# Optimization experiments

Measured on AMD Instinct MI355X. Metric: run time of the kernel, lower is better.

## Reference

```python
import jax, jax.numpy as jnp
import numpy as np

B, T, D, H, UNITS = 32, 2048, 512, 512, 512

def setup_inputs() -> dict:
    key = jax.random.key(0)
    ks = jax.random.split(key, 5)
    scale = 0.02
    return {
        "features": jax.random.normal(ks[0], (B, T, D), dtype=jnp.float32),
        "hidden": jax.random.normal(ks[1], (B, H), dtype=jnp.float32),
        "Wk": jax.random.normal(ks[2], (D, UNITS), dtype=jnp.float32) * scale,
        "Wb": jnp.zeros((UNITS,), dtype=jnp.float32),
        "Uk": jax.random.normal(ks[3], (H, UNITS), dtype=jnp.float32) * scale,
        "Ub": jnp.zeros((UNITS,), dtype=jnp.float32),
        "Vk": jax.random.normal(ks[4], (UNITS, 1), dtype=jnp.float32) * scale,
        "Vb": jnp.zeros((1,), dtype=jnp.float32),
    }

def reference(features, hidden, Wk, Wb, Uk, Ub, Vk, Vb):
    # features: [B, T, D], hidden: [B, H]
    wf = jnp.einsum('btd,du->btu', features, Wk) + Wb          # [B, T, U]
    uh = (hidden @ Uk + Ub)[:, None, :]                        # [B, 1, U]
    score = jnp.tanh(wf + uh)                                  # [B, T, U]
    logits = jnp.einsum('btu,uo->bto', score, Vk) + Vb         # [B, T, 1]
    attention_weights = jax.nn.softmax(logits, axis=1)         # [B, T, 1]
    context_vector = jnp.sum(attention_weights * features, axis=1)  # [B, D]
    return context_vector, attention_weights
```

## Files before the change

kernel.cpp:

```cpp
#include <hip/hip_runtime.h>
#include <stdint.h>


typedef unsigned short ushort_t;
typedef __attribute__((ext_vector_type(8))) short short8;
typedef __attribute__((ext_vector_type(4))) float f32x4;
typedef __attribute__((ext_vector_type(2))) float float2v;
typedef __attribute__((ext_vector_type(2))) __bf16 bf162v;

#define GLOBAL_AS __attribute__((address_space(1)))
#define LDS_AS    __attribute__((address_space(3)))

__device__ __forceinline__ ushort_t f2bf(float f) {
    uint32_t u = __builtin_bit_cast(uint32_t, f);
    u = (u + 0x7fffu + ((u >> 16) & 1u)) >> 16;
    return (ushort_t)u;
}
__device__ __forceinline__ uint32_t pkbf(float a, float b) {
    bf162v r = __builtin_convertvector((float2v){a, b}, bf162v);
    return __builtin_bit_cast(uint32_t, r);
}

__global__ __launch_bounds__(256) void prep_all(
    const float* __restrict__ hidden, const float* __restrict__ Uk,
    const float* __restrict__ Ub, const float* __restrict__ Wb,
    const float* __restrict__ Wk,
    float* __restrict__ uh, ushort_t* __restrict__ WkT)
{
    const int pb = blockIdx.x;
    if (pb < 256) {
        const int b  = pb >> 3;
        const int u  = (pb & 7) * 64 + (threadIdx.x & 63);
        const int k0 = (threadIdx.x >> 6) * 128;
        const float* hr = hidden + b * 512;
        float acc = 0.f;
        #pragma unroll 8
        for (int k = k0; k < k0 + 128; ++k)
            acc += hr[k] * Uk[k * 512 + u];
        __shared__ float red[256];
        red[threadIdx.x] = acc;
        __syncthreads();
        if (threadIdx.x < 64) {
            const int ul = threadIdx.x;
            uh[b * 512 + u] = red[ul] + red[ul + 64] + red[ul + 128] + red[ul + 192]
                            + Ub[u] + Wb[u];
        }
    } else {
        __shared__ float t[32][33];
        const int blk = pb - 256;
        const int ti = blk >> 4;
        const int tj = blk & 15;
        const int tx = threadIdx.x & 31;
        const int ty = threadIdx.x >> 5;
        #pragma unroll
        for (int q = 0; q < 4; ++q) {
            const int r = ty * 4 + q;
            t[r][tx] = Wk[(ti * 32 + r) * 512 + tj * 32 + tx];
        }
        __syncthreads();
        #pragma unroll
        for (int q = 0; q < 4; ++q) {
            const int r = ty * 4 + q;
            WkT[(tj * 32 + r) * 512 + ti * 32 + tx] = f2bf(t[tx][r]);
        }
    }
}

#define APAD 40
__global__ __launch_bounds__(1024, 4) void attn_gemm(
    const float* __restrict__ feats, const ushort_t* __restrict__ WkT,
    const float* __restrict__ uh, const float* __restrict__ Vk,
    float* __restrict__ lg)
{
    __shared__ __align__(16) short As[2][128 * APAD];
    __shared__ __align__(16) short Bs[2][512 * 32];
    __shared__ float uh_s[512];
    __shared__ float vk_s[512];
    __shared__ float lpart[8][128];

    const int tid  = threadIdx.x;
    const int lane = tid & 63;
    const int quad = lane >> 4;
    const int lc   = lane & 15;
    const int wave = tid >> 6;
    const int wm   = wave >> 3;
    const int wn   = wave & 7;
    const int m0   = blockIdx.x * 128;
    const int bidx = m0 >> 11;

    if (tid < 512) {
        uh_s[tid] = uh[bidx * 512 + tid];
        vk_s[tid] = Vk[tid];
    }

    const int rowA = tid >> 3;
    const int kAo  = (tid & 7) * 4;
    const int rB0  = tid >> 2;
    const int sB   = tid & 3;

    f32x4 acc[4][4];
    #pragma unroll
    for (int tm = 0; tm < 4; ++tm)
        #pragma unroll
        for (int tn = 0; tn < 4; ++tn)
            acc[tm][tn] = (f32x4){0.f, 0.f, 0.f, 0.f};

    {
        #pragma unroll
        for (int rnd = 0; rnd < 2; ++rnd) {
            const int li = rnd * 1024 + tid;
            const int rB = rnd * 256 + rB0;
            const int kq = (sB ^ ((rB >> 1) & 3)) * 8;
            const ushort_t* gb = WkT + (size_t)rB * 512 + kq;
            __builtin_amdgcn_global_load_lds(
                (const GLOBAL_AS void*)gb, (LDS_AS void*)(Bs[0] + li * 8), 16, 0, 0);
        }
        const f32x4 av = *(const f32x4*)(feats + (size_t)(m0 + rowA) * 512 + kAo);
        uint2 w;
        w.x = pkbf(av.x, av.y);
        w.y = pkbf(av.z, av.w);
        *(uint2*)(As[0] + rowA * APAD + kAo) = w;
    }

    const int swzR = (lc >> 1) & 3;

    int buf = 0;
    for (int ks = 0; ks < 16; ++ks) {
        __syncthreads();

        f32x4 a_next;
        const bool have = (ks + 1) < 16;
        if (have) {
            const int k0n = (ks + 1) * 32;
            #pragma unroll
            for (int rnd = 0; rnd < 2; ++rnd) {
                const int li = rnd * 1024 + tid;
                const int rB = rnd * 256 + rB0;
                const int kq = (sB ^ ((rB >> 1) & 3)) * 8;
                const ushort_t* gb = WkT + (size_t)rB * 512 + k0n + kq;
                __builtin_amdgcn_global_load_lds(
                    (const GLOBAL_AS void*)gb, (LDS_AS void*)(Bs[buf ^ 1] + li * 8),
                    16, 0, 0);
            }
            a_next = *(const f32x4*)(feats + (size_t)(m0 + rowA) * 512 + k0n + kAo);
        }

        short8 af[4], bfr[4];
        #pragma unroll
        for (int t4 = 0; t4 < 4; ++t4) {
            af[t4]  = *(const short8*)(As[buf] + (wm * 64 + t4 * 16 + lc) * APAD + quad * 8);
            bfr[t4] = *(const short8*)(Bs[buf] + (wn * 64 + t4 * 16 + lc) * 32
                                       + ((quad ^ swzR) * 8));
        }
        #pragma unroll
        for (int tm = 0; tm < 4; ++tm)
            #pragma unroll
            for (int tn = 0; tn < 4; ++tn)
                acc[tm][tn] = __builtin_amdgcn_mfma_f32_16x16x32_bf16(
                    af[tm], bfr[tn], acc[tm][tn], 0, 0, 0);

        if (have) {
            uint2 w;
            w.x = pkbf(a_next.x, a_next.y);
            w.y = pkbf(a_next.z, a_next.w);
            *(uint2*)(As[buf ^ 1] + rowA * APAD + kAo) = w;
        }
        buf ^= 1;
    }

    float rp[16];
    #pragma unroll
    for (int i = 0; i < 16; ++i) rp[i] = 0.f;
    #pragma unroll
    for (int tn = 0; tn < 4; ++tn) {
        const int nl  = wn * 64 + tn * 16 + lc;
        const float uhv = uh_s[nl];
        const float vkv = vk_s[nl];
        #pragma unroll
        for (int tm = 0; tm < 4; ++tm)
            #pragma unroll
            for (int i = 0; i < 4; ++i) {
                const float x = acc[tm][tn][i] + uhv;
                const float e = __expf(2.0f * x);
                rp[tm * 4 + i] += (1.0f - 2.0f / (e + 1.0f)) * vkv;
            }
    }
    #pragma unroll
    for (int i = 0; i < 16; ++i) {
        float v = rp[i];
        v += __shfl_xor(v, 1, 64);
        v += __shfl_xor(v, 2, 64);
        v += __shfl_xor(v, 4, 64);
        v += __shfl_xor(v, 8, 64);
        rp[i] = v;
    }
    if (lc == 0) {
        #pragma unroll
        for (int tm = 0; tm < 4; ++tm)
            #pragma unroll
            for (int i = 0; i < 4; ++i)
                lpart[wn][wm * 64 + tm * 16 + quad * 4 + i] = rp[tm * 4 + i];
    }
    __syncthreads();
    if (tid < 128) {
        float s = 0.f;
        #pragma unroll
        for (int j = 0; j < 8; ++j) s += lpart[j][tid];
        lg[m0 + tid] = s;
    }
}

__global__ __launch_bounds__(256) void softmax_k(
    const float* __restrict__ lg, float* __restrict__ aw_out)
{
    const int b = blockIdx.x, tid = threadIdx.x;
    const float* p = lg + b * 2048;
    float v[8];
    #pragma unroll
    for (int i = 0; i < 8; ++i) v[i] = p[tid + i * 256];
    float mx = -1e30f;
    #pragma unroll
    for (int i = 0; i < 8; ++i) mx = fmaxf(mx, v[i]);
    #pragma unroll
    for (int off = 32; off >= 1; off >>= 1) mx = fmaxf(mx, __shfl_xor(mx, off, 64));
    __shared__ float redm[4], reds[4];
    const int wv = tid >> 6, ln = tid & 63;
    if (ln == 0) redm[wv] = mx;
    __syncthreads();
    mx = fmaxf(fmaxf(redm[0], redm[1]), fmaxf(redm[2], redm[3]));
    float s = 0.f;
    #pragma unroll
    for (int i = 0; i < 8; ++i) { v[i] = __expf(v[i] - mx); s += v[i]; }
    #pragma unroll
    for (int off = 32; off >= 1; off >>= 1) s += __shfl_xor(s, off, 64);
    if (ln == 0) reds[wv] = s;
    __syncthreads();
    s = reds[0] + reds[1] + reds[2] + reds[3];
    const float inv = 1.0f / s;
    #pragma unroll
    for (int i = 0; i < 8; ++i)
        aw_out[b * 2048 + tid + i * 256] = v[i] * inv;
}

__global__ __launch_bounds__(256) void context_part(
    const float* __restrict__ feats, const float* __restrict__ aw,
    float* __restrict__ part)
{
    const int b     = blockIdx.x >> 4;
    const int chunk = blockIdx.x & 15;
    const int half  = threadIdx.x >> 7;
    const int t0    = chunk * 128 + half * 64;
    const int d4    = (threadIdx.x & 127) * 4;
    const float* wp = aw + b * 2048 + t0;
    const float* fp = feats + (size_t)(b * 2048 + t0) * 512 + d4;
    f32x4 a = (f32x4){0.f, 0.f, 0.f, 0.f};
    #pragma unroll 4
    for (int tt = 0; tt < 64; ++tt) {
        const float w = wp[tt];
        const f32x4 f = *(const f32x4*)(fp + (size_t)tt * 512);
        a.x += w * f.x; a.y += w * f.y; a.z += w * f.z; a.w += w * f.w;
    }
    *(f32x4*)(part + (size_t)(b * 32 + chunk * 2 + half) * 512 + d4) = a;
}

__global__ __launch_bounds__(512) void context_reduce(
    const float* __restrict__ part, float* __restrict__ ctx)
{
    const int b = blockIdx.x;
    const int d = threadIdx.x;
    const float* p = part + (size_t)b * 32 * 512 + d;
    float s = 0.f;
    #pragma unroll
    for (int j = 0; j < 32; ++j) s += p[j * 512];
    ctx[b * 512 + d] = s;
}

extern "C" void kernel_launch(void* const* d_in, const int* in_sizes, int n_in,
                              void* d_out, int out_size, void* d_ws, size_t ws_size,
                              hipStream_t stream)
{
    const float* feats  = (const float*)d_in[0];
    const float* hidden = (const float*)d_in[1];
    const float* Wk     = (const float*)d_in[2];
    const float* Wb     = (const float*)d_in[3];
    const float* Uk     = (const float*)d_in[4];
    const float* Ub     = (const float*)d_in[5];
    const float* Vk     = (const float*)d_in[6];

    float* out       = (float*)d_out;
    float* ctx_out_p = out;
    float* aw_out_p  = out + 16384;

    char* ws = (char*)d_ws;
    float*    uh   = (float*)ws;
    ushort_t* WkT  = (ushort_t*)(ws + 65536);
    float*    lg   = (float*)(ws + 589824);
    float*    part = (float*)(ws + 851968);

    prep_all      <<<512, 256, 0, stream>>>(hidden, Uk, Ub, Wb, Wk, uh, WkT);
    attn_gemm     <<<512, 1024, 0, stream>>>(feats, WkT, uh, Vk, lg);
    softmax_k     <<<32,  256, 0, stream>>>(lg, aw_out_p);
    context_part  <<<512, 256, 0, stream>>>(feats, aw_out_p, part);
    context_reduce<<<32,  512, 0, stream>>>(part, ctx_out_p);
}
```

Measured before the change: 257.4 us.

## Triple-buffer Wk tiles with manual vmcnt waits to prefetch two stages ahead

Turns the B-operand (WkT) LDS staging from double to triple buffering, so the direct global-to-LDS loads are issued two k-steps ahead and rotated through three buffers. The __syncthreads is replaced by an explicit s_waitcnt vmcnt(2) plus s_barrier, letting one stage of loads stay in flight across the barrier. The aim is to hide global load latency behind the MFMA work. In exchange it uses another 32KB of LDS, which may lower occupancy, and it relies on a hand-counted vmcnt that also has to cover the A-feature register loads.

```diff
diff --git a/kernel.cpp b/kernel.cpp
--- a/kernel.cpp
+++ b/kernel.cpp
@@ -73,7 +73,7 @@
     float* __restrict__ lg)
 {
     __shared__ __align__(16) short As[2][128 * APAD];
-    __shared__ __align__(16) short Bs[2][512 * 32];
+    __shared__ __align__(16) short Bs_all[3][512 * 32];
     __shared__ float uh_s[512];
     __shared__ float vk_s[512];
     __shared__ float lpart[8][128];
@@ -97,6 +97,7 @@
     const int kAo  = (tid & 7) * 4;
     const int rB0  = tid >> 2;
     const int sB   = tid & 3;
+    const int kqB  = (sB ^ ((rB0 >> 1) & 3)) * 8;
 
     f32x4 acc[4][4];
     #pragma unroll
@@ -105,17 +106,25 @@
         for (int tn = 0; tn < 4; ++tn)
             acc[tm][tn] = (f32x4){0.f, 0.f, 0.f, 0.f};
 
+    short* Brd  = Bs_all[0];
+    short* Bmid = Bs_all[1];
+    short* Bwr  = Bs_all[2];
+
     {
-        #pragma unroll
-        for (int rnd = 0; rnd < 2; ++rnd) {
-            const int li = rnd * 1024 + tid;
-            const int rB = rnd * 256 + rB0;
-            const int kq = (sB ^ ((rB >> 1) & 3)) * 8;
-            const ushort_t* gb = WkT + (size_t)rB * 512 + kq;
-            __builtin_amdgcn_global_load_lds(
-                (const GLOBAL_AS void*)gb, (LDS_AS void*)(Bs[0] + li * 8), 16, 0, 0);
-        }
         const f32x4 av = *(const f32x4*)(feats + (size_t)(m0 + rowA) * 512 + kAo);
+        #pragma unroll
+        for (int pt = 0; pt < 2; ++pt) {
+            short* dst = (pt == 0) ? Brd : Bmid;
+            #pragma unroll
+            for (int rnd = 0; rnd < 2; ++rnd) {
+                const int li = rnd * 1024 + tid;
+                const int rB = rnd * 256 + rB0;
+                const int kq = (sB ^ ((rB >> 1) & 3)) * 8;
+                const ushort_t* gb = WkT + (size_t)rB * 512 + pt * 32 + kq;
+                __builtin_amdgcn_global_load_lds(
+                    (const GLOBAL_AS void*)gb, (LDS_AS void*)(dst + li * 8), 16, 0, 0);
+            }
+        }
         uint2 w;
         w.x = pkbf(av.x, av.y);
         w.y = pkbf(av.z, av.w);
@@ -126,12 +135,21 @@
 
     int buf = 0;
     for (int ks = 0; ks < 16; ++ks) {
-        __syncthreads();
+        if (ks < 15) {
+            asm volatile("s_waitcnt vmcnt(2) lgkmcnt(0)" ::: "memory");
+        } else {
+            asm volatile("s_waitcnt vmcnt(0) lgkmcnt(0)" ::: "memory");
+        }
+        __builtin_amdgcn_s_barrier();
 
         f32x4 a_next;
-        const bool have = (ks + 1) < 16;
-        if (have) {
-            const int k0n = (ks + 1) * 32;
+        const bool haveA = (ks + 1) < 16;
+        if (haveA)
+            a_next = *(const f32x4*)(feats + (size_t)(m0 + rowA) * 512
+                                     + (ks + 1) * 32 + kAo);
+
+        if (ks + 2 < 16) {
+            const int k0n = (ks + 2) * 32;
             #pragma unroll
             for (int rnd = 0; rnd < 2; ++rnd) {
                 const int li = rnd * 1024 + tid;
@@ -139,17 +157,15 @@
                 const int kq = (sB ^ ((rB >> 1) & 3)) * 8;
                 const ushort_t* gb = WkT + (size_t)rB * 512 + k0n + kq;
                 __builtin_amdgcn_global_load_lds(
-                    (const GLOBAL_AS void*)gb, (LDS_AS void*)(Bs[buf ^ 1] + li * 8),
-                    16, 0, 0);
+                    (const GLOBAL_AS void*)gb, (LDS_AS void*)(Bwr + li * 8), 16, 0, 0);
             }
-            a_next = *(const f32x4*)(feats + (size_t)(m0 + rowA) * 512 + k0n + kAo);
         }
 
         short8 af[4], bfr[4];
         #pragma unroll
         for (int t4 = 0; t4 < 4; ++t4) {
             af[t4]  = *(const short8*)(As[buf] + (wm * 64 + t4 * 16 + lc) * APAD + quad * 8);
-            bfr[t4] = *(const short8*)(Bs[buf] + (wn * 64 + t4 * 16 + lc) * 32
+            bfr[t4] = *(const short8*)(Brd + (wn * 64 + t4 * 16 + lc) * 32
                                        + ((quad ^ swzR) * 8));
         }
         #pragma unroll
@@ -159,13 +175,15 @@
                 acc[tm][tn] = __builtin_amdgcn_mfma_f32_16x16x32_bf16(
                     af[tm], bfr[tn], acc[tm][tn], 0, 0, 0);
 
-        if (have) {
+        if (haveA) {
             uint2 w;
             w.x = pkbf(a_next.x, a_next.y);
             w.y = pkbf(a_next.z, a_next.w);
             *(uint2*)(As[buf ^ 1] + rowA * APAD + kAo) = w;
         }
         buf ^= 1;
+
+        short* t = Brd; Brd = Bmid; Bmid = Bwr; Bwr = t;
     }
 
     float rp[16];
```

Result: no change. 262.6 us (+2.0%).

## Deepen GEMM K-tile to 64 with XOR-swizzled LDS and interleaved MFMA phases

Applied to the files above, without the earlier changes.

Doubles the K step of the attention GEMM to 64, halving the number of main-loop iterations and block-wide barriers. Both LDS tiles switch to an XOR swizzle in place of padding. Each iteration is split into four MFMA phases separated by s_barrier and sched_barrier, with the global-to-LDS loads for the next tile spread across them and s_setprio raised around MFMA bursts. LDS use rises to about 160KB per 1024-thread block, and the extra barriers plus moving uh/Vk into direct global reads could offset the gains.

```diff
diff --git a/kernel.cpp b/kernel.cpp
--- a/kernel.cpp
+++ b/kernel.cpp
@@ -5,6 +5,7 @@
 typedef unsigned short ushort_t;
 typedef __attribute__((ext_vector_type(8))) short short8;
 typedef __attribute__((ext_vector_type(4))) float f32x4;
+typedef __attribute__((ext_vector_type(4))) uint32_t u32x4;
 typedef __attribute__((ext_vector_type(2))) float float2v;
 typedef __attribute__((ext_vector_type(2))) __bf16 bf162v;
 
@@ -66,17 +67,14 @@
     }
 }
 
-#define APAD 40
+#define MFMA_B16(a, b, c) __builtin_amdgcn_mfma_f32_16x16x32_bf16(a, b, c, 0, 0, 0)
 __global__ __launch_bounds__(1024, 4) void attn_gemm(
     const float* __restrict__ feats, const ushort_t* __restrict__ WkT,
     const float* __restrict__ uh, const float* __restrict__ Vk,
     float* __restrict__ lg)
 {
-    __shared__ __align__(16) short As[2][128 * APAD];
-    __shared__ __align__(16) short Bs[2][512 * 32];
-    __shared__ float uh_s[512];
-    __shared__ float vk_s[512];
-    __shared__ float lpart[8][128];
+    __shared__ __align__(16) short As[2][128 * 64];
+    __shared__ __align__(16) short Bs[2][512 * 64];
 
     const int tid  = threadIdx.x;
     const int lane = tid & 63;
@@ -88,15 +86,36 @@
     const int m0   = blockIdx.x * 128;
     const int bidx = m0 >> 11;
 
-    if (tid < 512) {
-        uh_s[tid] = uh[bidx * 512 + tid];
-        vk_s[tid] = Vk[tid];
+    int ofsA[4][2], ofsB[4][2];
+    #pragma unroll
+    for (int m = 0; m < 4; ++m) {
+        const int r = wm * 64 + m * 16 + lc;
+        #pragma unroll
+        for (int h = 0; h < 2; ++h)
+            ofsA[m][h] = r * 128 + (((h * 4 + quad) ^ (r & 7)) * 16);
+    }
+    #pragma unroll
+    for (int n = 0; n < 4; ++n) {
+        const int r = wn * 64 + n * 16 + lc;
+        #pragma unroll
+        for (int h = 0; h < 2; ++h)
+            ofsB[n][h] = r * 128 + (((h * 4 + quad) ^ (r & 7)) * 16);
     }
 
     const int rowA = tid >> 3;
-    const int kAo  = (tid & 7) * 4;
-    const int rB0  = tid >> 2;
-    const int sB   = tid & 3;
+    const int cA   = tid & 7;
+    const int dstA = rowA * 128 + ((cA ^ (rowA & 7)) * 16);
+    const float* apb = feats + (size_t)(m0 + rowA) * 512 + cA * 8;
+
+    int srcB[4], dstB[4];
+    #pragma unroll
+    for (int rnd = 0; rnd < 4; ++rnd) {
+        const int li = rnd * 1024 + tid;
+        const int rB = li >> 3;
+        const int sB = tid & 7;
+        srcB[rnd] = rB * 512 + ((sB ^ (rB & 7)) * 8);
+        dstB[rnd] = li * 16;
+    }
 
     f32x4 acc[4][4];
     #pragma unroll
@@ -107,82 +126,134 @@
 
     {
         #pragma unroll
-        for (int rnd = 0; rnd < 2; ++rnd) {
-            const int li = rnd * 1024 + tid;
-            const int rB = rnd * 256 + rB0;
-            const int kq = (sB ^ ((rB >> 1) & 3)) * 8;
-            const ushort_t* gb = WkT + (size_t)rB * 512 + kq;
-            __builtin_amdgcn_global_load_lds(
-                (const GLOBAL_AS void*)gb, (LDS_AS void*)(Bs[0] + li * 8), 16, 0, 0);
-        }
-        const f32x4 av = *(const f32x4*)(feats + (size_t)(m0 + rowA) * 512 + kAo);
-        uint2 w;
-        w.x = pkbf(av.x, av.y);
-        w.y = pkbf(av.z, av.w);
-        *(uint2*)(As[0] + rowA * APAD + kAo) = w;
-    }
-
-    const int swzR = (lc >> 1) & 3;
+        for (int rnd = 0; rnd < 4; ++rnd)
+            __builtin_amdgcn_global_load_lds(
+                (const GLOBAL_AS void*)(WkT + srcB[rnd]),
+                (LDS_AS void*)((char*)Bs[0] + dstB[rnd]), 16, 0, 0);
+        const f32x4 a0 = *(const f32x4*)(apb);
+        const f32x4 a1 = *(const f32x4*)(apb + 4);
+        u32x4 w = (u32x4){pkbf(a0.x, a0.y), pkbf(a0.z, a0.w),
+                          pkbf(a1.x, a1.y), pkbf(a1.z, a1.w)};
+        *(u32x4*)((char*)As[0] + dstA) = w;
+    }
 
     int buf = 0;
-    for (int ks = 0; ks < 16; ++ks) {
+    for (int ks = 0; ks < 8; ++ks) {
         __syncthreads();
-
-        f32x4 a_next;
-        const bool have = (ks + 1) < 16;
+        const short* Ab = As[buf];
+        const short* Bb = Bs[buf];
+        short* Bn = Bs[buf ^ 1];
+        const bool have = (ks + 1) < 8;
+
+        f32x4 an0, an1;
         if (have) {
-            const int k0n = (ks + 1) * 32;
-            #pragma unroll
-            for (int rnd = 0; rnd < 2; ++rnd) {
-                const int li = rnd * 1024 + tid;
-                const int rB = rnd * 256 + rB0;
-                const int kq = (sB ^ ((rB >> 1) & 3)) * 8;
-                const ushort_t* gb = WkT + (size_t)rB * 512 + k0n + kq;
-                __builtin_amdgcn_global_load_lds(
-                    (const GLOBAL_AS void*)gb, (LDS_AS void*)(Bs[buf ^ 1] + li * 8),
-                    16, 0, 0);
-            }
-            a_next = *(const f32x4*)(feats + (size_t)(m0 + rowA) * 512 + k0n + kAo);
-        }
-
-        short8 af[4], bfr[4];
-        #pragma unroll
-        for (int t4 = 0; t4 < 4; ++t4) {
-            af[t4]  = *(const short8*)(As[buf] + (wm * 64 + t4 * 16 + lc) * APAD + quad * 8);
-            bfr[t4] = *(const short8*)(Bs[buf] + (wn * 64 + t4 * 16 + lc) * 32
-                                       + ((quad ^ swzR) * 8));
-        }
-        #pragma unroll
-        for (int tm = 0; tm < 4; ++tm)
-            #pragma unroll
-            for (int tn = 0; tn < 4; ++tn)
-                acc[tm][tn] = __builtin_amdgcn_mfma_f32_16x16x32_bf16(
-                    af[tm], bfr[tn], acc[tm][tn], 0, 0, 0);
-
+            an0 = *(const f32x4*)(apb + (ks + 1) * 64);
+            an1 = *(const f32x4*)(apb + (ks + 1) * 64 + 4);
+        }
+
+        short8 bf0[4], af0, af1;
+        #pragma unroll
+        for (int n = 0; n < 4; ++n)
+            bf0[n] = *(const short8*)((const char*)Bb + ofsB[n][0]);
+        af0 = *(const short8*)((const char*)Ab + ofsA[0][0]);
+        af1 = *(const short8*)((const char*)Ab + ofsA[1][0]);
         if (have) {
-            uint2 w;
-            w.x = pkbf(a_next.x, a_next.y);
-            w.y = pkbf(a_next.z, a_next.w);
-            *(uint2*)(As[buf ^ 1] + rowA * APAD + kAo) = w;
+            const int kb = (ks + 1) * 64;
+            __builtin_amdgcn_global_load_lds(
+                (const GLOBAL_AS void*)(WkT + kb + srcB[0]),
+                (LDS_AS void*)((char*)Bn + dstB[0]), 16, 0, 0);
+            __builtin_amdgcn_global_load_lds(
+                (const GLOBAL_AS void*)(WkT + kb + srcB[1]),
+                (LDS_AS void*)((char*)Bn + dstB[1]), 16, 0, 0);
+        }
+        __builtin_amdgcn_sched_barrier(0);
+        __builtin_amdgcn_s_barrier();
+        __builtin_amdgcn_s_setprio(1);
+        #pragma unroll
+        for (int n = 0; n < 4; ++n) {
+            acc[0][n] = MFMA_B16(af0, bf0[n], acc[0][n]);
+            acc[1][n] = MFMA_B16(af1, bf0[n], acc[1][n]);
+        }
+        __builtin_amdgcn_s_setprio(0);
+        __builtin_amdgcn_sched_barrier(0);
+
+        short8 af2 = *(const short8*)((const char*)Ab + ofsA[2][0]);
+        short8 af3 = *(const short8*)((const char*)Ab + ofsA[3][0]);
+        if (have) {
+            const int kb = (ks + 1) * 64;
+            __builtin_amdgcn_global_load_lds(
+                (const GLOBAL_AS void*)(WkT + kb + srcB[2]),
+                (LDS_AS void*)((char*)Bn + dstB[2]), 16, 0, 0);
+            __builtin_amdgcn_global_load_lds(
+                (const GLOBAL_AS void*)(WkT + kb + srcB[3]),
+                (LDS_AS void*)((char*)Bn + dstB[3]), 16, 0, 0);
+        }
+        __builtin_amdgcn_sched_barrier(0);
+        __builtin_amdgcn_s_barrier();
+        __builtin_amdgcn_s_setprio(1);
+        #pragma unroll
+        for (int n = 0; n < 4; ++n) {
+            acc[2][n] = MFMA_B16(af2, bf0[n], acc[2][n]);
+            acc[3][n] = MFMA_B16(af3, bf0[n], acc[3][n]);
+        }
+        __builtin_amdgcn_s_setprio(0);
+        __builtin_amdgcn_sched_barrier(0);
+
+        short8 bf1[4], ag0, ag1;
+        #pragma unroll
+        for (int n = 0; n < 4; ++n)
+            bf1[n] = *(const short8*)((const char*)Bb + ofsB[n][1]);
+        ag0 = *(const short8*)((const char*)Ab + ofsA[0][1]);
+        ag1 = *(const short8*)((const char*)Ab + ofsA[1][1]);
+        __builtin_amdgcn_sched_barrier(0);
+        __builtin_amdgcn_s_barrier();
+        __builtin_amdgcn_s_setprio(1);
+        #pragma unroll
+        for (int n = 0; n < 4; ++n) {
+            acc[0][n] = MFMA_B16(ag0, bf1[n], acc[0][n]);
+            acc[1][n] = MFMA_B16(ag1, bf1[n], acc[1][n]);
+        }
+        __builtin_amdgcn_s_setprio(0);
+        __builtin_amdgcn_sched_barrier(0);
+
+        short8 ag2 = *(const short8*)((const char*)Ab + ofsA[2][1]);
+        short8 ag3 = *(const short8*)((const char*)Ab + ofsA[3][1]);
+        __builtin_amdgcn_sched_barrier(0);
+        __builtin_amdgcn_s_barrier();
+        __builtin_amdgcn_s_setprio(1);
+        #pragma unroll
+        for (int n = 0; n < 4; ++n) {
+            acc[2][n] = MFMA_B16(ag2, bf1[n], acc[2][n]);
+            acc[3][n] = MFMA_B16(ag3, bf1[n], acc[3][n]);
+        }
+        __builtin_amdgcn_s_setprio(0);
+        if (have) {
+            u32x4 w = (u32x4){pkbf(an0.x, an0.y), pkbf(an0.z, an0.w),
+                              pkbf(an1.x, an1.y), pkbf(an1.z, an1.w)};
+            *(u32x4*)((char*)As[buf ^ 1] + dstA) = w;
         }
         buf ^= 1;
     }
 
+    float uhv[4], vkv[4];
+    #pragma unroll
+    for (int tn = 0; tn < 4; ++tn) {
+        const int nl = wn * 64 + tn * 16 + lc;
+        uhv[tn] = uh[bidx * 512 + nl];
+        vkv[tn] = Vk[nl];
+    }
     float rp[16];
     #pragma unroll
     for (int i = 0; i < 16; ++i) rp[i] = 0.f;
     #pragma unroll
     for (int tn = 0; tn < 4; ++tn) {
-        const int nl  = wn * 64 + tn * 16 + lc;
-        const float uhv = uh_s[nl];
-        const float vkv = vk_s[nl];
         #pragma unroll
         for (int tm = 0; tm < 4; ++tm)
             #pragma unroll
             for (int i = 0; i < 4; ++i) {
-                const float x = acc[tm][tn][i] + uhv;
+                const float x = acc[tm][tn][i] + uhv[tn];
                 const float e = __expf(2.0f * x);
-                rp[tm * 4 + i] += (1.0f - 2.0f / (e + 1.0f)) * vkv;
+                rp[tm * 4 + i] += (1.0f - 2.0f / (e + 1.0f)) * vkv[tn];
             }
     }
     #pragma unroll
@@ -194,18 +265,20 @@
         v += __shfl_xor(v, 8, 64);
         rp[i] = v;
     }
+    __syncthreads();
+    float* lp = (float*)(&As[0][0]);
     if (lc == 0) {
         #pragma unroll
         for (int tm = 0; tm < 4; ++tm)
             #pragma unroll
             for (int i = 0; i < 4; ++i)
-                lpart[wn][wm * 64 + tm * 16 + quad * 4 + i] = rp[tm * 4 + i];
+                lp[wn * 128 + wm * 64 + tm * 16 + quad * 4 + i] = rp[tm * 4 + i];
     }
     __syncthreads();
     if (tid < 128) {
         float s = 0.f;
         #pragma unroll
-        for (int j = 0; j < 8; ++j) s += lpart[j][tid];
+        for (int j = 0; j < 8; ++j) s += lp[j * 128 + tid];
         lg[m0 + tid] = s;
     }
 }
```

After: 291.4 us. +13.2%, slower.
